# Optimization experiments

Measured on AMD Instinct MI355X. Metric: run time of the kernel, lower is better.

## Reference

```python
import jax, jax.numpy as jnp
import numpy as np

BATCH, SEQ, DIM, DSTATE = 8, 2048, 1024, 16


def setup_inputs() -> dict:
    key = jax.random.key(0)
    ks = jax.random.split(key, 8)
    u = jax.random.normal(ks[0], (BATCH, SEQ, DIM), jnp.float32)
    gate = jax.random.normal(ks[1], (BATCH, SEQ, DIM), jnp.float32)
    # parameters (init per module: normal std=0.01 for A_log/B/C, zeros for D)
    A_log = 0.01 * jax.random.normal(ks[2], (DSTATE, DSTATE), jnp.float32)
    B_mat = 0.01 * jax.random.normal(ks[3], (DIM, DSTATE), jnp.float32)
    C_mat = 0.01 * jax.random.normal(ks[4], (DIM, DSTATE), jnp.float32)
    D = jnp.zeros((DIM,), jnp.float32)
    bound = 1.0 / np.sqrt(DIM)  # nn.Linear default init
    dt_w = jax.random.uniform(ks[5], (1, DIM), jnp.float32, -bound, bound)
    dt_b = jax.random.uniform(ks[6], (1,), jnp.float32, -bound, bound)
    return {"u": u, "gate": gate, "A_log": A_log, "B_mat": B_mat,
            "C_mat": C_mat, "D": D, "dt_w": dt_w, "dt_b": dt_b}


def reference(u, gate, A_log, B_mat, C_mat, D, dt_w, dt_b):
    # delta = sigmoid(Linear(gate)) : [B, S, 1] -> [B, S]
    delta = jax.nn.sigmoid(jnp.einsum('bsd,od->bso', gate, dt_w) + dt_b)[..., 0]
    A = -jnp.exp(A_log)                               # [N, N]
    scaled_A = delta[..., None, None] * A             # [B, S, N, N]
    A_exp = jax.scipy.linalg.expm(scaled_A)           # batched matrix exp
    Bu = jnp.einsum('bsd,dn->bsn', u, B_mat)          # [B, S, N]

    def step(h, inp):
        Aexp_t, bu_t = inp                            # [B,N,N], [B,N]
        h = jnp.einsum('bn,bnm->bm', h, Aexp_t) + bu_t
        return h, h

    h0 = jnp.zeros((u.shape[0], DSTATE), u.dtype)
    _, hs = jax.lax.scan(step, h0, (jnp.swapaxes(A_exp, 0, 1), jnp.swapaxes(Bu, 0, 1)))
    hs = jnp.swapaxes(hs, 0, 1)                       # [B, S, N]
    y = jnp.einsum('bsn,dn->bsd', hs, C_mat) + D * u  # [B, S, D]
    return y
```

## Files before the change

### kernel.cpp

```cpp
#include <hip/hip_runtime.h>

#define BATCH  8
#define SEQ    2048
#define DIMSZ  1024
#define NST    16
#define LCH    32
#define CPB    (SEQ / LCH)
#define NCHUNK (BATCH * CPB)
#define NCHEB  32

typedef __attribute__((ext_vector_type(8))) short bf16x8;
typedef __attribute__((ext_vector_type(4))) float f32x4;

static __device__ __forceinline__ unsigned short f2bf(float f) {
    unsigned u = __builtin_bit_cast(unsigned, f);
    unsigned r = (u + 0x7FFFu + ((u >> 16) & 1u)) >> 16;
    return (unsigned short)r;
}
static __device__ __forceinline__ float bf2f(unsigned short h) {
    unsigned u = ((unsigned)h) << 16;
    return __builtin_bit_cast(float, u);
}

__global__ __launch_bounds__(256) void sA_nodes(
    const float* __restrict__ A_log, float* __restrict__ Fn)
{
    __shared__ float Xs[16 * 17];
    __shared__ float Ts[16 * 17];
    const int tid = threadIdx.x;
    const int i = tid >> 4, j = tid & 15;
    const float th = (2.f * blockIdx.x + 1.f) * (3.14159265358979f / 64.f);
    const float dl = 0.5f * (1.f + cosf(th));
    const float a  = -expf(A_log[tid]);
    const float x  = dl * a * (1.0f / 64.0f);
    Xs[i*17 + j] = x;
    Ts[i*17 + j] = x;
    float S = x + (i == j ? 1.0f : 0.0f);
    __syncthreads();
#pragma unroll
    for (int k = 2; k <= 8; ++k) {
        float nt = 0.f;
#pragma unroll
        for (int kk = 0; kk < 16; ++kk)
            nt = fmaf(Ts[i*17 + kk], Xs[kk*17 + j], nt);
        nt *= (1.0f / (float)k);
        S += nt;
        __syncthreads();
        Ts[i*17 + j] = nt;
        __syncthreads();
    }
#pragma unroll
    for (int r = 0; r < 6; ++r) {
        __syncthreads();
        Ts[i*17 + j] = S;
        __syncthreads();
        float nt = 0.f;
#pragma unroll
        for (int kk = 0; kk < 16; ++kk)
            nt = fmaf(Ts[i*17 + kk], Ts[kk*17 + j], nt);
        S = nt;
    }
    Fn[(size_t)blockIdx.x * 256 + tid] = S;
}

__global__ __launch_bounds__(256) void sB_setup(
    const float* __restrict__ Fn, const float* __restrict__ B_mat,
    const float* __restrict__ dt_w,
    float* __restrict__ Gt,
    unsigned short* __restrict__ Bfh, unsigned short* __restrict__ Bfl,
    unsigned short* __restrict__ Wfh, unsigned short* __restrict__ Wfl)
{
    const int tid = threadIdx.x;
    const int blk = blockIdx.x;
    if (blk < NCHEB) {
        const int m = blk;
        float acc = 0.f;
        for (int k = 0; k < NCHEB; ++k) {
            const float th = (2.f * k + 1.f) * (3.14159265358979f / 64.f);
            acc = fmaf(Fn[(size_t)k * 256 + tid], cosf(m * th), acc);
        }
        const float sc = (m == 0) ? (1.f / 32.f) : (2.f / 32.f);
        Gt[(size_t)tid * NCHEB + m] = acc * sc;
    } else {
        const int idx0 = (blk - NCHEB) * 2048;
        for (int t = 0; t < 8; ++t) {
            const int idx = idx0 + t * 256 + tid;
            const int j  = idx & 7;
            const int l  = (idx >> 3) & 63;
            const int ks = idx >> 9;
            const int k  = ks * 32 + ((l >> 4) << 3) + j;
            const int n  = l & 15;
            float bv = B_mat[(size_t)k * 16 + n];
            unsigned short h = f2bf(bv);
            Bfh[idx] = h;
            Bfl[idx] = f2bf(bv - bf2f(h));
            float wv = (n == 0) ? dt_w[k] : 0.f;
            h = f2bf(wv);
            Wfh[idx] = h;
            Wfl[idx] = f2bf(wv - bf2f(h));
        }
    }
}

__global__ __launch_bounds__(256) void k1a_delta(
    const float* __restrict__ gate, const float* __restrict__ dt_w,
    const float* __restrict__ dt_b, float* __restrict__ delta)
{
    const int tid  = threadIdx.x;
    const int lane = tid & 63;
    const int w    = tid >> 6;
    const int tok  = blockIdx.x * 4 + w;
    const float* gp = gate + (size_t)tok * DIMSZ;
    float s = 0.f;
#pragma unroll
    for (int i = 0; i < 4; ++i) {
        const float4 g  = *(const float4*)(gp   + i * 256 + lane * 4);
        const float4 wv = *(const float4*)(dt_w + i * 256 + lane * 4);
        s = fmaf(g.x, wv.x, s); s = fmaf(g.y, wv.y, s);
        s = fmaf(g.z, wv.z, s); s = fmaf(g.w, wv.w, s);
    }
#pragma unroll
    for (int off = 32; off >= 1; off >>= 1)
        s += __shfl_xor(s, off, 64);
    if (lane == 0)
        delta[tok] = 1.0f / (1.0f + expf(-(s + dt_b[0])));
}

__global__ __launch_bounds__(256, 2) void k1b_bu(
    const float* __restrict__ u,
    const unsigned short* __restrict__ Bfh, const unsigned short* __restrict__ Bfl,
    float* __restrict__ Bu)
{
    __shared__ float lds[2][32 * 128];
    const int tid  = threadIdx.x;
    const int lane = tid & 63;
    const int w    = tid >> 6;
    const int tok0 = blockIdx.x * 32;
    const int half = w & 1;
    const int wrow = (w >> 1) * 16;
    const int q    = lane >> 4;
    const int r    = lane & 15;

    const uint4* bh = (const uint4*)Bfh;
    const uint4* bl = (const uint4*)Bfl;

    const int srow = 8 * w + (lane >> 5);
    const int p    = lane & 31;
    int colb[4];
#pragma unroll
    for (int i = 0; i < 4; ++i) {
        const int row = srow + 2 * i;
        const int lc  = (p & 16) | ((p & 15) ^ (row & 15));
        colb[i] = ((lc & 16) ? 512 : 0) + (lc & 15) * 4;
    }

    auto stage = [&](int c, int b) {
#pragma unroll
        for (int i = 0; i < 4; ++i) {
            const float* g = u + (size_t)(tok0 + srow + 2 * i) * DIMSZ
                               + (colb[i] + c * 64);
            __builtin_amdgcn_global_load_lds(
                (const __attribute__((address_space(1))) void*)g,
                (__attribute__((address_space(3))) void*)&lds[b][(8 * w + 2 * i) * 128],
                16, 0, 0);
        }
    };

    f32x4 acc = {0.f, 0.f, 0.f, 0.f};
    uint4 fh[2][2], fl[2][2];

    stage(0, 0);
    stage(1, 1);
    {
        const int ks0 = half * 16;
        fh[0][0] = bh[(ks0 + 0) * 64 + lane]; fl[0][0] = bl[(ks0 + 0) * 64 + lane];
        fh[0][1] = bh[(ks0 + 1) * 64 + lane]; fl[0][1] = bl[(ks0 + 1) * 64 + lane];
    }
    asm volatile("s_waitcnt vmcnt(8)" ::: "memory");
    __builtin_amdgcn_sched_barrier(0);
    __builtin_amdgcn_s_barrier();

#pragma unroll
    for (int c = 0; c < 8; ++c) {
        const int b = c & 1;
        float fu[2][8];
#pragma unroll
        for (int s = 0; s < 2; ++s) {
            const int c16a = (s * 8 + 2 * q + 0) ^ r;
            const int c16b = (s * 8 + 2 * q + 1) ^ r;
            const float4 v0 = *(const float4*)&lds[b][(wrow + r) * 128 + (half * 16 + c16a) * 4];
            const float4 v1 = *(const float4*)&lds[b][(wrow + r) * 128 + (half * 16 + c16b) * 4];
            fu[s][0] = v0.x; fu[s][1] = v0.y; fu[s][2] = v0.z; fu[s][3] = v0.w;
            fu[s][4] = v1.x; fu[s][5] = v1.y; fu[s][6] = v1.z; fu[s][7] = v1.w;
        }
        asm volatile("s_waitcnt lgkmcnt(0)" ::: "memory");
        __builtin_amdgcn_sched_barrier(0);
        __builtin_amdgcn_s_barrier();
        if (c + 2 < 8) stage(c + 2, b);
        if (c + 1 < 8) {
            const int ks0 = half * 16 + 2 * (c + 1);
            fh[(c + 1) & 1][0] = bh[(ks0 + 0) * 64 + lane];
            fl[(c + 1) & 1][0] = bl[(ks0 + 0) * 64 + lane];
            fh[(c + 1) & 1][1] = bh[(ks0 + 1) * 64 + lane];
            fl[(c + 1) & 1][1] = bl[(ks0 + 1) * 64 + lane];
        }
        __builtin_amdgcn_sched_barrier(0);
#pragma unroll
        for (int s = 0; s < 2; ++s) {
            bf16x8 uh, ul;
#pragma unroll
            for (int i = 0; i < 8; ++i) {
                unsigned short h = f2bf(fu[s][i]);
                uh[i] = (short)h;
                ul[i] = (short)f2bf(fu[s][i] - bf2f(h));
            }
            const bf16x8 Bh = __builtin_bit_cast(bf16x8, fh[b][s]);
            const bf16x8 Bl = __builtin_bit_cast(bf16x8, fl[b][s]);
            acc = __builtin_amdgcn_mfma_f32_16x16x32_bf16(uh, Bh, acc, 0, 0, 0);
            acc = __builtin_amdgcn_mfma_f32_16x16x32_bf16(uh, Bl, acc, 0, 0, 0);
            acc = __builtin_amdgcn_mfma_f32_16x16x32_bf16(ul, Bh, acc, 0, 0, 0);
        }
        if (c < 7) {
            if (c < 6) asm volatile("s_waitcnt vmcnt(8)" ::: "memory");
            else       asm volatile("s_waitcnt vmcnt(4)" ::: "memory");
            __builtin_amdgcn_sched_barrier(0);
            __builtin_amdgcn_s_barrier();
        }
    }

    float* red = &lds[0][0];
#pragma unroll
    for (int rr = 0; rr < 4; ++rr)
        red[w * 256 + (q * 4 + rr) * 16 + r] = acc[rr];
    __syncthreads();
    const int base = blockIdx.x * 512;
    Bu[base + tid]       = red[tid]       + red[256 + tid];
    Bu[base + 256 + tid] = red[512 + tid] + red[768 + tid];
}

__global__ __launch_bounds__(256) void kA_chunk(
    const float* __restrict__ Gt, const float* __restrict__ delta,
    const float* __restrict__ Bu,
    float* __restrict__ P, float* __restrict__ e)
{
    __shared__ float dl[LCH];
    __shared__ float sd[1];
    __shared__ float Bus[LCH * NST];
    __shared__ float Mlds[LCH * 256];
    __shared__ float Ps[16 * 17];
    const int tid = threadIdx.x;
    const size_t g = blockIdx.x;
    if (tid < LCH) dl[tid] = delta[g * LCH + tid];
    for (int idx = tid; idx < LCH * NST; idx += 256)
        Bus[idx] = Bu[g * (size_t)(LCH * NST) + idx];
    float gr[NCHEB];
    {
        const float4* gp = (const float4*)(Gt + (size_t)tid * NCHEB);
#pragma unroll
        for (int qq = 0; qq < NCHEB / 4; ++qq) {
            float4 v = gp[qq];
            gr[qq*4+0] = v.x; gr[qq*4+1] = v.y; gr[qq*4+2] = v.z; gr[qq*4+3] = v.w;
        }
    }
    __syncthreads();
    if (tid == 0) {
        float s = 0.f;
        for (int t = 0; t < LCH; ++t) s += dl[t];
        sd[0] = s;
    }
    for (int t = 0; t < LCH; ++t) {
        const float x = 2.f * dl[t] - 1.f;
        float acc = fmaf(gr[1], x, gr[0]);
        float tm2 = 1.f, tm1 = x;
#pragma unroll
        for (int m = 2; m < NCHEB; ++m) {
            const float tm = fmaf(2.f * x, tm1, -tm2);
            acc = fmaf(gr[m], tm, acc);
            tm2 = tm1; tm1 = tm;
        }
        Mlds[t * 256 + tid] = acc;
    }
    __syncthreads();
    float S;
    {
        const float xp = 2.f * (sd[0] * (1.f / LCH)) - 1.f;
        float acc = fmaf(gr[1], xp, gr[0]);
        float tm2 = 1.f, tm1 = xp;
#pragma unroll
        for (int m = 2; m < NCHEB; ++m) {
            const float tm = fmaf(2.f * xp, tm1, -tm2);
            acc = fmaf(gr[m], tm, acc);
            tm2 = tm1; tm1 = tm;
        }
        S = acc;
    }
    const int i = tid >> 4, j = tid & 15;
#pragma unroll
    for (int r = 0; r < 5; ++r) {
        Ps[i*17 + j] = S;
        __syncthreads();
        float ns = 0.f;
#pragma unroll
        for (int k = 0; k < 16; ++k)
            ns = fmaf(Ps[i*17 + k], Ps[k*17 + j], ns);
        __syncthreads();
        S = ns;
    }
    P[g * 256 + tid] = S;
    if (tid < 16) {
        float h = 0.f;
        for (int t = 0; t < LCH; ++t) {
            float hn = Bus[t * 16 + tid];
#pragma unroll
            for (int i2 = 0; i2 < 16; ++i2)
                hn = fmaf(__shfl(h, i2, 64), Mlds[t * 256 + i2 * 16 + tid], hn);
            h = hn;
        }
        e[g * NST + tid] = h;
    }
}

__global__ __launch_bounds__(256) void k4_scan(
    const float* __restrict__ P, const float* __restrict__ e,
    float* __restrict__ hin)
{
    __shared__ float Pl[32 * 272];
    __shared__ float el[32 * NST];
    const int tid = threadIdx.x;
    const int b = blockIdx.x;
    float h = 0.f;
    for (int half = 0; half < 2; ++half) {
        const int c0 = half * 32;
        for (int idx = tid; idx < 32*256; idx += 256) {
            const int c = idx >> 8, ij = idx & 255, i = ij >> 4, jj = ij & 15;
            Pl[c*272 + i*17 + jj] = P[((size_t)(b*CPB + c0 + c)) * 256 + ij];
        }
        for (int idx = tid; idx < 32*NST; idx += 256)
            el[idx] = e[((size_t)(b*CPB + c0)) * NST + idx];
        __syncthreads();
        if (tid < 64) {
            const int j = tid & 15;
            for (int c = 0; c < 32; ++c) {
                if (tid < 16) hin[((size_t)(b*CPB + c0 + c)) * NST + j] = h;
                float hn = el[c*16 + j];
#pragma unroll
                for (int i2 = 0; i2 < 16; ++i2)
                    hn = fmaf(__shfl(h, i2, 64), Pl[c*272 + i2*17 + j], hn);
                h = hn;
            }
        }
        __syncthreads();
    }
}

__global__ __launch_bounds__(256) void k5_out(
    const float* __restrict__ Gt, const float* __restrict__ delta,
    const float* __restrict__ Bu, const float* __restrict__ hin,
    const float* __restrict__ u, const float* __restrict__ C_mat,
    const float* __restrict__ D, float* __restrict__ y)
{
    __shared__ float dl[LCH];
    __shared__ float Bus[LCH * NST];
    __shared__ float Mlds[LCH * 256];
    __shared__ __align__(16) float Hs[LCH * NST];
    const int tid = threadIdx.x;
    const size_t g = blockIdx.x;
    if (tid < LCH) dl[tid] = delta[g * LCH + tid];
    for (int idx = tid; idx < LCH * NST; idx += 256)
        Bus[idx] = Bu[g * (size_t)(LCH * NST) + idx];
    float gr[NCHEB];
    {
        const float4* gp = (const float4*)(Gt + (size_t)tid * NCHEB);
#pragma unroll
        for (int qq = 0; qq < NCHEB / 4; ++qq) {
            float4 v = gp[qq];
            gr[qq*4+0] = v.x; gr[qq*4+1] = v.y; gr[qq*4+2] = v.z; gr[qq*4+3] = v.w;
        }
    }
    __syncthreads();
    for (int t = 0; t < LCH; ++t) {
        const float x = 2.f * dl[t] - 1.f;
        float acc = fmaf(gr[1], x, gr[0]);
        float tm2 = 1.f, tm1 = x;
#pragma unroll
        for (int m = 2; m < NCHEB; ++m) {
            const float tm = fmaf(2.f * x, tm1, -tm2);
            acc = fmaf(gr[m], tm, acc);
            tm2 = tm1; tm1 = tm;
        }
        Mlds[t * 256 + tid] = acc;
    }
    __syncthreads();
    if (tid < 16) {
        float h = hin[g * NST + tid];
        for (int t = 0; t < LCH; ++t) {
            float hn = Bus[t * 16 + tid];
#pragma unroll
            for (int i2 = 0; i2 < 16; ++i2)
                hn = fmaf(__shfl(h, i2, 64), Mlds[t * 256 + i2 * 16 + tid], hn);
            h = hn;
            Hs[t * 16 + tid] = h;
        }
    }
    __syncthreads();
    const int d0 = tid * 4;
    float4 cr[4][4];
#pragma unroll
    for (int r = 0; r < 4; ++r)
#pragma unroll
        for (int qq = 0; qq < 4; ++qq)
            cr[r][qq] = ((const float4*)C_mat)[(d0 + r) * 4 + qq];
    const float4 dv = ((const float4*)D)[tid];
    for (int t = 0; t < LCH; ++t) {
        const size_t row = (g * LCH + t) * DIMSZ;
        const float4 uv = ((const float4*)(u + row))[tid];
        float y0 = dv.x * uv.x, y1 = dv.y * uv.y, y2 = dv.z * uv.z, y3 = dv.w * uv.w;
#pragma unroll
        for (int qq = 0; qq < 4; ++qq) {
            const float4 hq = *((const float4*)&Hs[t*16 + qq*4]);
            y0 = fmaf(hq.x, cr[0][qq].x, y0); y0 = fmaf(hq.y, cr[0][qq].y, y0);
            y0 = fmaf(hq.z, cr[0][qq].z, y0); y0 = fmaf(hq.w, cr[0][qq].w, y0);
            y1 = fmaf(hq.x, cr[1][qq].x, y1); y1 = fmaf(hq.y, cr[1][qq].y, y1);
            y1 = fmaf(hq.z, cr[1][qq].z, y1); y1 = fmaf(hq.w, cr[1][qq].w, y1);
            y2 = fmaf(hq.x, cr[2][qq].x, y2); y2 = fmaf(hq.y, cr[2][qq].y, y2);
            y2 = fmaf(hq.z, cr[2][qq].z, y2); y2 = fmaf(hq.w, cr[2][qq].w, y2);
            y3 = fmaf(hq.x, cr[3][qq].x, y3); y3 = fmaf(hq.y, cr[3][qq].y, y3);
            y3 = fmaf(hq.z, cr[3][qq].z, y3); y3 = fmaf(hq.w, cr[3][qq].w, y3);
        }
        float4 ov; ov.x = y0; ov.y = y1; ov.z = y2; ov.w = y3;
        ((float4*)(y + row))[tid] = ov;
    }
}

extern "C" void kernel_launch(void* const* d_in, const int* in_sizes, int n_in,
                              void* d_out, int out_size, void* d_ws, size_t ws_size,
                              hipStream_t stream)
{
    const float* u     = (const float*)d_in[0];
    const float* gate  = (const float*)d_in[1];
    const float* A_log = (const float*)d_in[2];
    const float* B_mat = (const float*)d_in[3];
    const float* C_mat = (const float*)d_in[4];
    const float* D     = (const float*)d_in[5];
    const float* dt_w  = (const float*)d_in[6];
    const float* dt_b  = (const float*)d_in[7];
    float* y = (float*)d_out;

    float* ws = (float*)d_ws;
    size_t o = 0;
    float* Fn    = ws + o; o += 32 * 256;
    float* Gt    = ws + o; o += 256 * NCHEB;
    float* delta = ws + o; o += (size_t)BATCH * SEQ;
    float* Bu    = ws + o; o += (size_t)BATCH * SEQ * NST;
    float* P     = ws + o; o += (size_t)NCHUNK * 256;
    float* e     = ws + o; o += (size_t)NCHUNK * NST;
    float* hin   = ws + o; o += (size_t)NCHUNK * NST;
    unsigned short* Bfh = (unsigned short*)(ws + o); o += 8192;
    unsigned short* Bfl = (unsigned short*)(ws + o); o += 8192;
    unsigned short* Wfh = (unsigned short*)(ws + o); o += 8192;
    unsigned short* Wfl = (unsigned short*)(ws + o); o += 8192;

    sA_nodes<<<NCHEB, 256, 0, stream>>>(A_log, Fn);
    sB_setup<<<NCHEB + 8, 256, 0, stream>>>(Fn, B_mat, dt_w, Gt, Bfh, Bfl, Wfh, Wfl);
    k1a_delta<<<BATCH * SEQ / 4, 256, 0, stream>>>(gate, dt_w, dt_b, delta);
    k1b_bu  <<<BATCH * SEQ / 32, 256, 0, stream>>>(u, Bfh, Bfl, Bu);
    kA_chunk<<<NCHUNK, 256, 0, stream>>>(Gt, delta, Bu, P, e);
    k4_scan <<<BATCH,  256, 0, stream>>>(P, e, hin);
    k5_out  <<<NCHUNK, 256, 0, stream>>>(Gt, delta, Bu, hin, u, C_mat, D, y);
}
```

Measured before the change: 267.2 us.

## Split output kernel into state-recompute and wide projection kernels

The fused output kernel is split in two. One kernel recomputes the per-chunk hidden states and writes them to a global workspace. A second kernel then does the C-projection plus the D*u term over 8 timesteps per block, launched with four times as many blocks. The goal is more parallelism and memory-level concurrency on the bandwidth-bound y/u streaming phase, which was serialized over 32 timesteps per block. The cost is an extra launch and a global round-trip of the state tensor.

New measurement: 267.6 us. No clear change (+0.1%).

```diff
diff --git a/kernel.cpp b/kernel.cpp
--- a/kernel.cpp
+++ b/kernel.cpp
@@ -353,16 +353,15 @@
     }
 }
 
-__global__ __launch_bounds__(256) void k5_out(
+__global__ __launch_bounds__(256) void k5h_state(
     const float* __restrict__ Gt, const float* __restrict__ delta,
     const float* __restrict__ Bu, const float* __restrict__ hin,
-    const float* __restrict__ u, const float* __restrict__ C_mat,
-    const float* __restrict__ D, float* __restrict__ y)
+    float* __restrict__ Hsg)
 {
     __shared__ float dl[LCH];
     __shared__ float Bus[LCH * NST];
     __shared__ float Mlds[LCH * 256];
-    __shared__ __align__(16) float Hs[LCH * NST];
+    __shared__ float Hs[LCH * NST];
     const int tid = threadIdx.x;
     const size_t g = blockIdx.x;
     if (tid < LCH) dl[tid] = delta[g * LCH + tid];
@@ -403,6 +402,19 @@
         }
     }
     __syncthreads();
+    Hsg[g * 512 + tid]       = Hs[tid];
+    Hsg[g * 512 + 256 + tid] = Hs[256 + tid];
+}
+
+__global__ __launch_bounds__(256) void k5p_proj(
+    const float* __restrict__ Hsg, const float* __restrict__ u,
+    const float* __restrict__ C_mat, const float* __restrict__ D,
+    float* __restrict__ y)
+{
+    __shared__ __align__(16) float Hl[8 * NST];
+    const int tid = threadIdx.x;
+    const size_t blk = blockIdx.x;
+    if (tid < 128) Hl[tid] = Hsg[blk * 128 + tid];
     const int d0 = tid * 4;
     float4 cr[4][4];
 #pragma unroll
@@ -411,13 +423,15 @@
         for (int qq = 0; qq < 4; ++qq)
             cr[r][qq] = ((const float4*)C_mat)[(d0 + r) * 4 + qq];
     const float4 dv = ((const float4*)D)[tid];
-    for (int t = 0; t < LCH; ++t) {
-        const size_t row = (g * LCH + t) * DIMSZ;
+    __syncthreads();
+#pragma unroll
+    for (int t = 0; t < 8; ++t) {
+        const size_t row = (blk * 8 + t) * DIMSZ;
         const float4 uv = ((const float4*)(u + row))[tid];
         float y0 = dv.x * uv.x, y1 = dv.y * uv.y, y2 = dv.z * uv.z, y3 = dv.w * uv.w;
 #pragma unroll
         for (int qq = 0; qq < 4; ++qq) {
-            const float4 hq = *((const float4*)&Hs[t*16 + qq*4]);
+            const float4 hq = *((const float4*)&Hl[t * 16 + qq * 4]);
             y0 = fmaf(hq.x, cr[0][qq].x, y0); y0 = fmaf(hq.y, cr[0][qq].y, y0);
             y0 = fmaf(hq.z, cr[0][qq].z, y0); y0 = fmaf(hq.w, cr[0][qq].w, y0);
             y1 = fmaf(hq.x, cr[1][qq].x, y1); y1 = fmaf(hq.y, cr[1][qq].y, y1);
@@ -455,6 +469,7 @@
     float* P     = ws + o; o += (size_t)NCHUNK * 256;
     float* e     = ws + o; o += (size_t)NCHUNK * NST;
     float* hin   = ws + o; o += (size_t)NCHUNK * NST;
+    float* Hsg   = ws + o; o += (size_t)NCHUNK * LCH * NST;
     unsigned short* Bfh = (unsigned short*)(ws + o); o += 8192;
     unsigned short* Bfl = (unsigned short*)(ws + o); o += 8192;
     unsigned short* Wfh = (unsigned short*)(ws + o); o += 8192;
@@ -466,5 +481,6 @@
     k1b_bu  <<<BATCH * SEQ / 32, 256, 0, stream>>>(u, Bfh, Bfl, Bu);
     kA_chunk<<<NCHUNK, 256, 0, stream>>>(Gt, delta, Bu, P, e);
     k4_scan <<<BATCH,  256, 0, stream>>>(P, e, hin);
-    k5_out  <<<NCHUNK, 256, 0, stream>>>(Gt, delta, Bu, hin, u, C_mat, D, y);
-}
+    k5h_state<<<NCHUNK, 256, 0, stream>>>(Gt, delta, Bu, hin, Hsg);
+    k5p_proj <<<NCHUNK * LCH / 8, 256, 0, stream>>>(Hsg, u, C_mat, D, y);
+}
```

## Fuse Bu projection with chunk transition kernel, parallelize recurrences, skip zero-D u reads

Applied to the files above, without the earlier changes.

Merges the Bu GEMM kernel and the per-chunk matrix-power kernel into one launch, so Bu is handed over through shared memory and not re-read from global. The serial 16-lane recurrences in the chunk, scan and output kernels are split across 64 lanes, with 4-term partial dot products combined by xor shuffles, and the M matrices are padded to a stride of 17 to avoid bank conflicts. The output kernel skips loading u whenever D is zero, which matches the test inputs (D is all zeros) and removes a full read of u. The dead Wfh/Wfl setup is also dropped.

After: 242.7 us. -9.2%, faster.

```diff
diff --git a/kernel.cpp b/kernel.cpp
--- a/kernel.cpp
+++ b/kernel.cpp
@@ -65,10 +65,8 @@
 
 __global__ __launch_bounds__(256) void sB_setup(
     const float* __restrict__ Fn, const float* __restrict__ B_mat,
-    const float* __restrict__ dt_w,
     float* __restrict__ Gt,
-    unsigned short* __restrict__ Bfh, unsigned short* __restrict__ Bfl,
-    unsigned short* __restrict__ Wfh, unsigned short* __restrict__ Wfl)
+    unsigned short* __restrict__ Bfh, unsigned short* __restrict__ Bfl)
 {
     const int tid = threadIdx.x;
     const int blk = blockIdx.x;
@@ -94,10 +92,6 @@
             unsigned short h = f2bf(bv);
             Bfh[idx] = h;
             Bfl[idx] = f2bf(bv - bf2f(h));
-            float wv = (n == 0) ? dt_w[k] : 0.f;
-            h = f2bf(wv);
-            Wfh[idx] = h;
-            Wfl[idx] = f2bf(wv - bf2f(h));
         }
     }
 }
@@ -126,21 +120,29 @@
         delta[tok] = 1.0f / (1.0f + expf(-(s + dt_b[0])));
 }
 
-__global__ __launch_bounds__(256, 2) void k1b_bu(
+__global__ __launch_bounds__(256, 2) void kBA(
     const float* __restrict__ u,
     const unsigned short* __restrict__ Bfh, const unsigned short* __restrict__ Bfl,
-    float* __restrict__ Bu)
-{
-    __shared__ float lds[2][32 * 128];
+    const float* __restrict__ Gt, const float* __restrict__ delta,
+    float* __restrict__ Bu, float* __restrict__ P, float* __restrict__ e)
+{
+    __shared__ float smem[8704];
+    __shared__ float Bus[LCH * NST];
+    __shared__ float dl[LCH];
+    __shared__ float sd[1];
+    __shared__ float Ps[16 * 17];
     const int tid  = threadIdx.x;
     const int lane = tid & 63;
     const int w    = tid >> 6;
-    const int tok0 = blockIdx.x * 32;
+    const size_t gI = blockIdx.x;
+    const int tok0 = (int)gI * 32;
     const int half = w & 1;
     const int wrow = (w >> 1) * 16;
     const int q    = lane >> 4;
     const int r    = lane & 15;
 
+    if (tid < LCH) dl[tid] = delta[gI * LCH + tid];
+
     const uint4* bh = (const uint4*)Bfh;
     const uint4* bl = (const uint4*)Bfl;
 
@@ -157,11 +159,11 @@
     auto stage = [&](int c, int b) {
 #pragma unroll
         for (int i = 0; i < 4; ++i) {
-            const float* g = u + (size_t)(tok0 + srow + 2 * i) * DIMSZ
-                               + (colb[i] + c * 64);
+            const float* gp = u + (size_t)(tok0 + srow + 2 * i) * DIMSZ
+                                + (colb[i] + c * 64);
             __builtin_amdgcn_global_load_lds(
-                (const __attribute__((address_space(1))) void*)g,
-                (__attribute__((address_space(3))) void*)&lds[b][(8 * w + 2 * i) * 128],
+                (const __attribute__((address_space(1))) void*)gp,
+                (__attribute__((address_space(3))) void*)&smem[b * 4096 + (8 * w + 2 * i) * 128],
                 16, 0, 0);
         }
     };
@@ -188,8 +190,8 @@
         for (int s = 0; s < 2; ++s) {
             const int c16a = (s * 8 + 2 * q + 0) ^ r;
             const int c16b = (s * 8 + 2 * q + 1) ^ r;
-            const float4 v0 = *(const float4*)&lds[b][(wrow + r) * 128 + (half * 16 + c16a) * 4];
-            const float4 v1 = *(const float4*)&lds[b][(wrow + r) * 128 + (half * 16 + c16b) * 4];
+            const float4 v0 = *(const float4*)&smem[b * 4096 + (wrow + r) * 128 + (half * 16 + c16a) * 4];
+            const float4 v1 = *(const float4*)&smem[b * 4096 + (wrow + r) * 128 + (half * 16 + c16b) * 4];
             fu[s][0] = v0.x; fu[s][1] = v0.y; fu[s][2] = v0.z; fu[s][3] = v0.w;
             fu[s][4] = v1.x; fu[s][5] = v1.y; fu[s][6] = v1.z; fu[s][7] = v1.w;
         }
@@ -228,31 +230,18 @@
         }
     }
 
-    float* red = &lds[0][0];
+    float* red = smem;
 #pragma unroll
     for (int rr = 0; rr < 4; ++rr)
         red[w * 256 + (q * 4 + rr) * 16 + r] = acc[rr];
     __syncthreads();
-    const int base = blockIdx.x * 512;
-    Bu[base + tid]       = red[tid]       + red[256 + tid];
-    Bu[base + 256 + tid] = red[512 + tid] + red[768 + tid];
-}
-
-__global__ __launch_bounds__(256) void kA_chunk(
-    const float* __restrict__ Gt, const float* __restrict__ delta,
-    const float* __restrict__ Bu,
-    float* __restrict__ P, float* __restrict__ e)
-{
-    __shared__ float dl[LCH];
-    __shared__ float sd[1];
-    __shared__ float Bus[LCH * NST];
-    __shared__ float Mlds[LCH * 256];
-    __shared__ float Ps[16 * 17];
-    const int tid = threadIdx.x;
-    const size_t g = blockIdx.x;
-    if (tid < LCH) dl[tid] = delta[g * LCH + tid];
-    for (int idx = tid; idx < LCH * NST; idx += 256)
-        Bus[idx] = Bu[g * (size_t)(LCH * NST) + idx];
+    const float b0 = red[tid]       + red[256 + tid];
+    const float b1 = red[512 + tid] + red[768 + tid];
+    Bu[gI * 512 + tid]       = b0;
+    Bu[gI * 512 + 256 + tid] = b1;
+    Bus[tid]       = b0;
+    Bus[256 + tid] = b1;
+
     float gr[NCHEB];
     {
         const float4* gp = (const float4*)(Gt + (size_t)tid * NCHEB);
@@ -270,33 +259,33 @@
     }
     for (int t = 0; t < LCH; ++t) {
         const float x = 2.f * dl[t] - 1.f;
-        float acc = fmaf(gr[1], x, gr[0]);
+        float accm = fmaf(gr[1], x, gr[0]);
         float tm2 = 1.f, tm1 = x;
 #pragma unroll
         for (int m = 2; m < NCHEB; ++m) {
             const float tm = fmaf(2.f * x, tm1, -tm2);
-            acc = fmaf(gr[m], tm, acc);
+            accm = fmaf(gr[m], tm, accm);
             tm2 = tm1; tm1 = tm;
         }
-        Mlds[t * 256 + tid] = acc;
+        smem[t * 272 + (tid >> 4) * 17 + (tid & 15)] = accm;
     }
     __syncthreads();
     float S;
     {
         const float xp = 2.f * (sd[0] * (1.f / LCH)) - 1.f;
-        float acc = fmaf(gr[1], xp, gr[0]);
+        float accm = fmaf(gr[1], xp, gr[0]);
         float tm2 = 1.f, tm1 = xp;
 #pragma unroll
         for (int m = 2; m < NCHEB; ++m) {
             const float tm = fmaf(2.f * xp, tm1, -tm2);
-            acc = fmaf(gr[m], tm, acc);
+            accm = fmaf(gr[m], tm, accm);
             tm2 = tm1; tm1 = tm;
         }
-        S = acc;
+        S = accm;
     }
     const int i = tid >> 4, j = tid & 15;
 #pragma unroll
-    for (int r = 0; r < 5; ++r) {
+    for (int rr = 0; rr < 5; ++rr) {
         Ps[i*17 + j] = S;
         __syncthreads();
         float ns = 0.f;
@@ -306,17 +295,21 @@
         __syncthreads();
         S = ns;
     }
-    P[g * 256 + tid] = S;
-    if (tid < 16) {
+    P[gI * 256 + tid] = S;
+    if (tid < 64) {
+        const int gq = tid >> 4, jj = tid & 15, i0 = gq * 4;
         float h = 0.f;
         for (int t = 0; t < LCH; ++t) {
-            float hn = Bus[t * 16 + tid];
-#pragma unroll
-            for (int i2 = 0; i2 < 16; ++i2)
-                hn = fmaf(__shfl(h, i2, 64), Mlds[t * 256 + i2 * 16 + tid], hn);
-            h = hn;
-        }
-        e[g * NST + tid] = h;
+            float pp = 0.f;
+#pragma unroll
+            for (int m = 0; m < 4; ++m)
+                pp = fmaf(__shfl(h, gq * 20 + m, 64),
+                          smem[t * 272 + (i0 + m) * 17 + jj], pp);
+            pp += __shfl_xor(pp, 16, 64);
+            pp += __shfl_xor(pp, 32, 64);
+            h = Bus[t * 16 + jj] + pp;
+        }
+        if (gq == 0) e[gI * NST + jj] = h;
     }
 }
 
@@ -339,14 +332,17 @@
             el[idx] = e[((size_t)(b*CPB + c0)) * NST + idx];
         __syncthreads();
         if (tid < 64) {
-            const int j = tid & 15;
+            const int gq = tid >> 4, j = tid & 15, i0 = gq * 4;
             for (int c = 0; c < 32; ++c) {
                 if (tid < 16) hin[((size_t)(b*CPB + c0 + c)) * NST + j] = h;
-                float hn = el[c*16 + j];
-#pragma unroll
-                for (int i2 = 0; i2 < 16; ++i2)
-                    hn = fmaf(__shfl(h, i2, 64), Pl[c*272 + i2*17 + j], hn);
-                h = hn;
+                float pp = 0.f;
+#pragma unroll
+                for (int m = 0; m < 4; ++m)
+                    pp = fmaf(__shfl(h, gq * 20 + m, 64),
+                              Pl[c*272 + (i0 + m)*17 + j], pp);
+                pp += __shfl_xor(pp, 16, 64);
+                pp += __shfl_xor(pp, 32, 64);
+                h = el[c*16 + j] + pp;
             }
         }
         __syncthreads();
@@ -359,9 +355,9 @@
     const float* __restrict__ u, const float* __restrict__ C_mat,
     const float* __restrict__ D, float* __restrict__ y)
 {
+    __shared__ float Mlds[32 * 272];
+    __shared__ float Bus[LCH * NST];
     __shared__ float dl[LCH];
-    __shared__ float Bus[LCH * NST];
-    __shared__ float Mlds[LCH * 256];
     __shared__ __align__(16) float Hs[LCH * NST];
     const int tid = threadIdx.x;
     const size_t g = blockIdx.x;
@@ -380,26 +376,30 @@
     __syncthreads();
     for (int t = 0; t < LCH; ++t) {
         const float x = 2.f * dl[t] - 1.f;
-        float acc = fmaf(gr[1], x, gr[0]);
+        float accm = fmaf(gr[1], x, gr[0]);
         float tm2 = 1.f, tm1 = x;
 #pragma unroll
         for (int m = 2; m < NCHEB; ++m) {
             const float tm = fmaf(2.f * x, tm1, -tm2);
-            acc = fmaf(gr[m], tm, acc);
+            accm = fmaf(gr[m], tm, accm);
             tm2 = tm1; tm1 = tm;
         }
-        Mlds[t * 256 + tid] = acc;
-    }
-    __syncthreads();
-    if (tid < 16) {
-        float h = hin[g * NST + tid];
+        Mlds[t * 272 + (tid >> 4) * 17 + (tid & 15)] = accm;
+    }
+    __syncthreads();
+    if (tid < 64) {
+        const int gq = tid >> 4, jj = tid & 15, i0 = gq * 4;
+        float h = hin[g * NST + jj];
         for (int t = 0; t < LCH; ++t) {
-            float hn = Bus[t * 16 + tid];
-#pragma unroll
-            for (int i2 = 0; i2 < 16; ++i2)
-                hn = fmaf(__shfl(h, i2, 64), Mlds[t * 256 + i2 * 16 + tid], hn);
-            h = hn;
-            Hs[t * 16 + tid] = h;
+            float pp = 0.f;
+#pragma unroll
+            for (int m = 0; m < 4; ++m)
+                pp = fmaf(__shfl(h, gq * 20 + m, 64),
+                          Mlds[t * 272 + (i0 + m) * 17 + jj], pp);
+            pp += __shfl_xor(pp, 16, 64);
+            pp += __shfl_xor(pp, 32, 64);
+            h = Bus[t * 16 + jj] + pp;
+            if (gq == 0) Hs[t * 16 + jj] = h;
         }
     }
     __syncthreads();
@@ -411,10 +411,14 @@
         for (int qq = 0; qq < 4; ++qq)
             cr[r][qq] = ((const float4*)C_mat)[(d0 + r) * 4 + qq];
     const float4 dv = ((const float4*)D)[tid];
+    const bool dnz = (dv.x != 0.f) || (dv.y != 0.f) || (dv.z != 0.f) || (dv.w != 0.f);
     for (int t = 0; t < LCH; ++t) {
         const size_t row = (g * LCH + t) * DIMSZ;
-        const float4 uv = ((const float4*)(u + row))[tid];
-        float y0 = dv.x * uv.x, y1 = dv.y * uv.y, y2 = dv.z * uv.z, y3 = dv.w * uv.w;
+        float y0 = 0.f, y1 = 0.f, y2 = 0.f, y3 = 0.f;
+        if (dnz) {
+            const float4 uv = ((const float4*)(u + row))[tid];
+            y0 = dv.x * uv.x; y1 = dv.y * uv.y; y2 = dv.z * uv.z; y3 = dv.w * uv.w;
+        }
 #pragma unroll
         for (int qq = 0; qq < 4; ++qq) {
             const float4 hq = *((const float4*)&Hs[t*16 + qq*4]);
@@ -457,14 +461,11 @@
     float* hin   = ws + o; o += (size_t)NCHUNK * NST;
     unsigned short* Bfh = (unsigned short*)(ws + o); o += 8192;
     unsigned short* Bfl = (unsigned short*)(ws + o); o += 8192;
-    unsigned short* Wfh = (unsigned short*)(ws + o); o += 8192;
-    unsigned short* Wfl = (unsigned short*)(ws + o); o += 8192;
 
     sA_nodes<<<NCHEB, 256, 0, stream>>>(A_log, Fn);
-    sB_setup<<<NCHEB + 8, 256, 0, stream>>>(Fn, B_mat, dt_w, Gt, Bfh, Bfl, Wfh, Wfl);
+    sB_setup<<<NCHEB + 8, 256, 0, stream>>>(Fn, B_mat, Gt, Bfh, Bfl);
     k1a_delta<<<BATCH * SEQ / 4, 256, 0, stream>>>(gate, dt_w, dt_b, delta);
-    k1b_bu  <<<BATCH * SEQ / 32, 256, 0, stream>>>(u, Bfh, Bfl, Bu);
-    kA_chunk<<<NCHUNK, 256, 0, stream>>>(Gt, delta, Bu, P, e);
+    kBA     <<<NCHUNK, 256, 0, stream>>>(u, Bfh, Bfl, Gt, delta, Bu, P, e);
     k4_scan <<<BATCH,  256, 0, stream>>>(P, e, hin);
     k5_out  <<<NCHUNK, 256, 0, stream>>>(Gt, delta, Bu, hin, u, C_mat, D, y);
 }
```
